# Performance work log

Hardware: AMD Instinct MI355X
Metric: run time of the kernel (lower is better)

## Reference

```python
import jax, jax.numpy as jnp
import numpy as np

B, NPG, K, F_IN, H = 64, 256, 100, 5, 128  # graphs, nodes/graph, knn k, in feats, hidden
N = B * NPG
H2 = 6 * H
SLOPE = 0.01  # leaky_relu default
EPS = 1e-5    # batchnorm eps


def _leaky(x):
    return jnp.where(x > 0, x, SLOPE * x)


def _knn_edges(x):
    # knn_graph(x, K, batch), loop=False, flow=source_to_target: edges j->i for the
    # K nearest neighbors j of node i within the same graph.
    xb = x.reshape(B, NPG, F_IN)
    d2 = jnp.sum((xb[:, :, None, :] - xb[:, None, :, :]) ** 2, axis=-1)  # [B,NPG,NPG]
    d2 = d2 + jnp.eye(NPG, dtype=d2.dtype) * 1e10  # exclude self
    _, idx = jax.lax.top_k(-d2, K)  # [B,NPG,K] local neighbor ids
    offs = (jnp.arange(B) * NPG)[:, None, None]
    src = (idx + offs).reshape(-1)
    dst = jnp.broadcast_to(jnp.arange(NPG)[None, :, None] + offs, (B, NPG, K)).reshape(-1)
    return src, dst


def _tagconv(x, src, dst, norm, Ws, b):
    # PyG TAGConv: out = sum_k lin_k(L^k x), L = D^-1/2 A D^-1/2 (no self loops)
    out = x @ Ws[0]
    h = x
    for k in range(1, Ws.shape[0]):
        msg = h[src] * norm[:, None]                      # gather [E,F]
        h = jax.ops.segment_sum(msg, dst, num_segments=N)  # scatter-add
        out = out + h @ Ws[k]
    return out + b


def _pool(x, batch):
    cnt = jax.ops.segment_sum(jnp.ones((N,), x.dtype), batch, num_segments=B)
    mean = jax.ops.segment_sum(x, batch, num_segments=B) / cnt[:, None]
    mx = jax.ops.segment_max(x, batch, num_segments=B)
    return jnp.concatenate([mean, mx], axis=1)  # [B, 2F]


def reference(x, batch, conv1_w, conv1_b, conv2_w, conv2_b, conv3_w, conv3_b,
              bn_gamma, bn_beta, lin_w, lin_b, out_w, out_b):
    src, dst = _knn_edges(x)
    # gcn_norm: deg from target side, symmetric scaling
    deg = jax.ops.segment_sum(jnp.ones(src.shape, x.dtype), dst, num_segments=N)
    dinv = jnp.where(deg > 0, deg ** -0.5, 0.0)
    norm = dinv[src] * dinv[dst]

    h = _leaky(_tagconv(x, src, dst, norm, conv1_w, conv1_b))
    p1 = _pool(h, batch)
    h = _leaky(_tagconv(h, src, dst, norm, conv2_w, conv2_b))
    p2 = _pool(h, batch)
    h = _leaky(_tagconv(h, src, dst, norm, conv3_w, conv3_b))
    p3 = _pool(h, batch)

    g = jnp.concatenate([p1, p2, p3], axis=1)  # [B, 768]
    mu = jnp.mean(g, axis=0)
    var = jnp.mean((g - mu) ** 2, axis=0)
    g = (g - mu) * jax.lax.rsqrt(var + EPS) * bn_gamma + bn_beta

    for i in range(5):
        g = _leaky(g @ lin_w[i] + lin_b[i])
    return (g @ out_w + out_b).reshape(-1)


def setup_inputs() -> dict:
    key = jax.random.key(0)
    ks = jax.random.split(key, 16)
    x = jax.random.normal(ks[0], (N, F_IN), jnp.float32)
    batch = jnp.repeat(jnp.arange(B, dtype=jnp.int32), NPG)

    def w(k, shape, fan_in):
        return jax.random.normal(k, shape, jnp.float32) * (1.0 / np.sqrt(fan_in))

    return {
        "x": x, "batch": batch,
        "conv1_w": w(ks[1], (3, F_IN, H), F_IN), "conv1_b": jnp.zeros((H,), jnp.float32),
        "conv2_w": w(ks[2], (3, H, H), H), "conv2_b": jnp.zeros((H,), jnp.float32),
        "conv3_w": w(ks[3], (3, H, H), H), "conv3_b": jnp.zeros((H,), jnp.float32),
        "bn_gamma": jnp.ones((H2,), jnp.float32), "bn_beta": jnp.zeros((H2,), jnp.float32),
        "lin_w": w(ks[4], (5, H2, H2), H2), "lin_b": jnp.zeros((5, H2), jnp.float32),
        "out_w": w(ks[5], (H2, 1), H2), "out_b": jnp.zeros((1,), jnp.float32),
    }
```

## Files before the change

### kernel.cpp

```cpp
#include <hip/hip_runtime.h>
#include <hip/hip_bf16.h>
#include <math.h>

#define NN 16384
#define BB 64
#define NPG 256
#define KNN 100
#define FIN 5
#define HH 128
#define H2 768
#define SLOPE 0.01f

typedef __bf16 bf16x8 __attribute__((ext_vector_type(8)));
typedef float f32x4 __attribute__((ext_vector_type(4)));

__device__ __forceinline__ int detect_bf(const void* gamma) {
    return ((const unsigned*)gamma)[0] == 0x3F803F80u;
}
__device__ __forceinline__ float loadin(const void* p, size_t i, int bf) {
    return bf ? __bfloat162float(((const __hip_bfloat16*)p)[i]) : ((const float*)p)[i];
}
template <typename T>
__device__ __forceinline__ float ldT(const T* p, size_t i) { return (float)p[i]; }
template <>
__device__ __forceinline__ float ldT<__hip_bfloat16>(const __hip_bfloat16* p, size_t i) {
    return __bfloat162float(p[i]);
}
__device__ __forceinline__ float4 ldT4(const float* p) { return *(const float4*)p; }
__device__ __forceinline__ float4 ldT4(const __hip_bfloat16* p) {
    ushort4 u = *(const ushort4*)p;
    return make_float4(__uint_as_float((unsigned)u.x << 16),
                       __uint_as_float((unsigned)u.y << 16),
                       __uint_as_float((unsigned)u.z << 16),
                       __uint_as_float((unsigned)u.w << 16));
}
__device__ __forceinline__ void stage_chunk(float* dst, const float* src, int n, int t) {
    const float4* s = (const float4*)src;
    float4* d = (float4*)dst;
    int n4 = n >> 2;
    for (int i = t; i < n4; i += 256) d[i] = s[i];
}
__device__ __forceinline__ void stage_chunk(float* dst, const __hip_bfloat16* src, int n, int t) {
    const ushort4* s = (const ushort4*)src;
    int n4 = n >> 2;
    for (int i = t; i < n4; i += 256) {
        ushort4 u = s[i];
        dst[i * 4 + 0] = __uint_as_float((unsigned)u.x << 16);
        dst[i * 4 + 1] = __uint_as_float((unsigned)u.y << 16);
        dst[i * 4 + 2] = __uint_as_float((unsigned)u.z << 16);
        dst[i * 4 + 3] = __uint_as_float((unsigned)u.w << 16);
    }
}

__device__ __forceinline__ unsigned enc_f(float f) {
    unsigned u = __float_as_uint(f);
    return (u & 0x80000000u) ? ~u : (u | 0x80000000u);
}
__device__ __forceinline__ float dec_f(unsigned u) {
    return __uint_as_float((u & 0x80000000u) ? (u & 0x7FFFFFFFu) : ~u);
}
__device__ __forceinline__ unsigned f2bf(float f) {
    unsigned u = __float_as_uint(f);
    unsigned r = 0x7fffu + ((u >> 16) & 1u);
    return (u + r) >> 16;
}
__device__ __forceinline__ void split1(float x, unsigned short& h, unsigned short& l) {
    unsigned u = __float_as_uint(x);
    unsigned hb = u & 0xFFFF0000u;
    h = (unsigned short)(hb >> 16);
    float rem = x - __uint_as_float(hb);
    l = (unsigned short)f2bf(rem);
}

__global__ __launch_bounds__(256) void knn_kernel(const void* __restrict__ x_in,
                                                  const void* gamma,
                                                  unsigned char* __restrict__ nbr,
                                                  float* __restrict__ g,
                                                  float* __restrict__ outf,
                                                  unsigned* __restrict__ done) {
    int blk = blockIdx.x;
    int bf = detect_bf(gamma);
    int b = blk >> 6;
    int wave = threadIdx.x >> 6;
    int lane = threadIdx.x & 63;
    int il = ((blk & 63) << 2) + wave;
    {
        int gi = blk * 256 + threadIdx.x;
        if (blk < 192 && gi < BB * H2) {
            int cm = gi & 255;
            g[gi] = (cm < 128) ? 0.0f : __uint_as_float(0x007FFFFFu);
        }
        if (blk == 0 && threadIdx.x < BB) {
            outf[threadIdx.x] = 0.0f;
            done[threadIdx.x] = 0u;
        }
    }
    __shared__ float xg[FIN * NPG];
    for (int idx = threadIdx.x; idx < NPG * FIN; idx += 256) {
        int node = idx / FIN, c = idx - node * FIN;
        xg[c * NPG + node] = loadin(x_in, (size_t)b * NPG * FIN + idx, bf);
    }
    __syncthreads();
    float dq[4] = {0.f, 0.f, 0.f, 0.f};
    #pragma unroll
    for (int c = 0; c < FIN; ++c) {
        float xi = xg[c * NPG + il];
        float4 xv = *(const float4*)&xg[c * NPG + lane * 4];
        float d0 = xi - xv.x, d1 = xi - xv.y, d2 = xi - xv.z, d3 = xi - xv.w;
        dq[0] += d0 * d0; dq[1] += d1 * d1; dq[2] += d2 * d2; dq[3] += d3 * d3;
    }
    unsigned long long kq[4];
    #pragma unroll
    for (int q = 0; q < 4; ++q) {
        int e = lane * 4 + q;
        float dd = (e == il) ? 1e30f : dq[q];
        kq[q] = ((unsigned long long)__float_as_uint(dd) << 32) | (unsigned)e;
    }
    #pragma unroll
    for (int kk = 2; kk <= NPG; kk <<= 1) {
        #pragma unroll
        for (int j = kk >> 1; j > 0; j >>= 1) {
            unsigned long long nk[4];
            if (j >= 4) {
                int lj = j >> 2;
                #pragma unroll
                for (int q = 0; q < 4; ++q) {
                    unsigned long long pk = __shfl_xor(kq[q], lj, 64);
                    int e = lane * 4 + q;
                    bool keepmin = (((e & j) == 0) == ((e & kk) == 0));
                    unsigned long long mn = kq[q] < pk ? kq[q] : pk;
                    unsigned long long mx = kq[q] < pk ? pk : kq[q];
                    nk[q] = keepmin ? mn : mx;
                }
            } else {
                #pragma unroll
                for (int q = 0; q < 4; ++q) {
                    unsigned long long pk = kq[q ^ j];
                    int e = lane * 4 + q;
                    bool keepmin = (((e & j) == 0) == ((e & kk) == 0));
                    unsigned long long mn = kq[q] < pk ? kq[q] : pk;
                    unsigned long long mx = kq[q] < pk ? pk : kq[q];
                    nk[q] = keepmin ? mn : mx;
                }
            }
            kq[0] = nk[0]; kq[1] = nk[1]; kq[2] = nk[2]; kq[3] = nk[3];
        }
    }
    if (lane < 25) {
        uchar4 o = make_uchar4((unsigned char)kq[0], (unsigned char)kq[1],
                               (unsigned char)kq[2], (unsigned char)kq[3]);
        *(uchar4*)&nbr[(size_t)(b * NPG + il) * KNN + lane * 4] = o;
    }
}

__global__ void agg5x2_kernel(const void* __restrict__ x_in, const void* gamma,
                              const unsigned char* __restrict__ nbr,
                              float* __restrict__ t5a, float* __restrict__ t5b, float nrm) {
    int b = blockIdx.x, i = threadIdx.x;
    int bf = detect_bf(gamma);
    __shared__ float xs[NPG * FIN];
    __shared__ float ys[NPG * FIN];
    for (int idx = threadIdx.x; idx < NPG * FIN; idx += 256)
        xs[idx] = loadin(x_in, (size_t)b * NPG * FIN + idx, bf);
    __syncthreads();
    const unsigned char* nb = nbr + (size_t)(b * NPG + i) * KNN;
    float a0=0.f, a1=0.f, a2=0.f, a3=0.f, a4=0.f;
    for (int k = 0; k < KNN; ++k) {
        int base = (int)nb[k] * FIN;
        a0 += xs[base+0]; a1 += xs[base+1]; a2 += xs[base+2];
        a3 += xs[base+3]; a4 += xs[base+4];
    }
    a0 *= nrm; a1 *= nrm; a2 *= nrm; a3 *= nrm; a4 *= nrm;
    size_t o = (size_t)(b * NPG + i) * FIN;
    t5a[o+0] = a0; t5a[o+1] = a1; t5a[o+2] = a2; t5a[o+3] = a3; t5a[o+4] = a4;
    ys[i*FIN+0] = a0; ys[i*FIN+1] = a1; ys[i*FIN+2] = a2;
    ys[i*FIN+3] = a3; ys[i*FIN+4] = a4;
    __syncthreads();
    a0=0.f; a1=0.f; a2=0.f; a3=0.f; a4=0.f;
    for (int k = 0; k < KNN; ++k) {
        int base = (int)nb[k] * FIN;
        a0 += ys[base+0]; a1 += ys[base+1]; a2 += ys[base+2];
        a3 += ys[base+3]; a4 += ys[base+4];
    }
    t5b[o+0] = nrm*a0; t5b[o+1] = nrm*a1; t5b[o+2] = nrm*a2;
    t5b[o+3] = nrm*a3; t5b[o+4] = nrm*a4;
}

__global__ __launch_bounds__(256) void agg_mfma_kernel(
        const float* __restrict__ hin, const unsigned char* __restrict__ nbr,
        float* __restrict__ hout, float nrm) {
    __shared__ __align__(16) unsigned short At[64 * 256];
    __shared__ __align__(16) unsigned short Ht[64 * 256];
    int t = threadIdx.x;
    int gph = blockIdx.x;
    int m0 = blockIdx.y * 64;
    int c0 = blockIdx.z * 64;
    {
        uint4 zz = make_uint4(0u, 0u, 0u, 0u);
        uint4* za = (uint4*)At;
        #pragma unroll
        for (int i = 0; i < 8; ++i) za[t + i * 256] = zz;
    }
    __syncthreads();
    for (int it = t; it < NPG * 4; it += 256) {
        int nq = it >> 4, c4 = it & 15;
        const float* src = &hin[((size_t)(gph * NPG + nq * 4)) * HH + c0 + c4 * 4];
        float4 v0 = *(const float4*)(src);
        float4 v1 = *(const float4*)(src + HH);
        float4 v2 = *(const float4*)(src + 2 * HH);
        float4 v3 = *(const float4*)(src + 3 * HH);
        #pragma unroll
        for (int j = 0; j < 4; ++j) {
            int c = c4 * 4 + j;
            ushort4 pk;
            pk.x = (unsigned short)f2bf((&v0.x)[j]);
            pk.y = (unsigned short)f2bf((&v1.x)[j]);
            pk.z = (unsigned short)f2bf((&v2.x)[j]);
            pk.w = (unsigned short)f2bf((&v3.x)[j]);
            unsigned off = (unsigned)((c * 512 + nq * 8) ^ ((c & 7) << 4));
            *(ushort4*)((char*)Ht + off) = pk;
        }
    }
    {
        int r = t >> 2, q = t & 3;
        const unsigned char* nb = nbr + ((size_t)(gph * NPG + m0 + r)) * KNN + q * 25;
        unsigned rbase = (unsigned)(r * 512);
        unsigned rswz = (unsigned)((r & 7) << 4);
        for (int j = 0; j < 25; ++j) {
            int col = (int)nb[j];
            *(unsigned short*)((char*)At + ((rbase + col * 2) ^ rswz)) = 0x3F80u;
        }
    }
    __syncthreads();
    int wv = t >> 6, lane = t & 63;
    unsigned kgb = (unsigned)((lane >> 4) * 16);
    unsigned swz = (unsigned)((lane & 7) << 4);
    unsigned abase = (unsigned)((wv * 16 + (lane & 15)) * 512) + kgb;
    f32x4 acc[4];
    #pragma unroll
    for (int nt = 0; nt < 4; ++nt) acc[nt] = (f32x4){0.f, 0.f, 0.f, 0.f};
    #pragma unroll
    for (int ks = 0; ks < 8; ++ks) {
        bf16x8 a = *(const bf16x8*)((char*)At + ((abase + ks * 64) ^ swz));
        #pragma unroll
        for (int nt = 0; nt < 4; ++nt) {
            unsigned bb = (unsigned)((nt * 16 + (lane & 15)) * 512) + kgb + ks * 64;
            bf16x8 bv = *(const bf16x8*)((char*)Ht + (bb ^ swz));
            acc[nt] = __builtin_amdgcn_mfma_f32_16x16x32_bf16(a, bv, acc[nt], 0, 0, 0);
        }
    }
    int rbase2 = m0 + wv * 16 + (lane >> 4) * 4;
    #pragma unroll
    for (int nt = 0; nt < 4; ++nt) {
        int col = c0 + nt * 16 + (lane & 15);
        #pragma unroll
        for (int reg = 0; reg < 4; ++reg) {
            int node = gph * NPG + rbase2 + reg;
            hout[(size_t)node * HH + col] = acc[nt][reg] * nrm;
        }
    }
}

__device__ __forceinline__ void pool_epilogue(float* g, int b, int gc0, int cg, int rp,
                                              float* sv, float* mv) {
    #pragma unroll
    for (int mask = 1; mask < 16; mask <<= 1) {
        #pragma unroll
        for (int i = 0; i < 8; ++i) {
            sv[i] += __shfl_xor(sv[i], mask);
            mv[i] = fmaxf(mv[i], __shfl_xor(mv[i], mask));
        }
    }
    if (rp == 0) {
        #pragma unroll
        for (int i = 0; i < 8; ++i) {
            atomicAdd(&g[(size_t)b * H2 + gc0 + cg * 8 + i], sv[i]);
            atomicMax((unsigned*)&g[(size_t)b * H2 + gc0 + HH + cg * 8 + i], enc_f(mv[i]));
        }
    }
}

template <typename T>
__device__ __forceinline__ void tagmm5_body(
        const T* __restrict__ X0raw, const float* __restrict__ X1,
        const float* __restrict__ X2,
        const T* __restrict__ W, const T* __restrict__ bias,
        float* __restrict__ O, float* g, float* Ws, float* Xs) {
    int t = threadIdx.x;
    int r0 = blockIdx.x * 16;
    int r = t & 15, cg = t >> 4;
    float acc[8] = {0.f,0.f,0.f,0.f,0.f,0.f,0.f,0.f};
    for (int h = 0; h < 3; ++h) {
        stage_chunk(Ws, W + (size_t)h * FIN * HH, FIN * HH, t);
        for (int idx = t; idx < 16 * FIN; idx += 256) {
            int rr = idx / FIN, k = idx - rr * FIN;
            size_t src = (size_t)(r0 + rr) * FIN + k;
            Xs[rr * 9 + k] = (h == 0) ? ldT(X0raw, src)
                           : (h == 1) ? X1[src] : X2[src];
        }
        __syncthreads();
        #pragma unroll
        for (int k = 0; k < FIN; ++k) {
            float xv = Xs[r * 9 + k];
            const float4 wa = *(const float4*)&Ws[k * HH + cg * 8];
            const float4 wb = *(const float4*)&Ws[k * HH + cg * 8 + 4];
            acc[0] += xv * wa.x; acc[1] += xv * wa.y;
            acc[2] += xv * wa.z; acc[3] += xv * wa.w;
            acc[4] += xv * wb.x; acc[5] += xv * wb.y;
            acc[6] += xv * wb.z; acc[7] += xv * wb.w;
        }
        __syncthreads();
    }
    size_t orow = (size_t)(r0 + r) * HH + cg * 8;
    float sv[8], mv[8];
    #pragma unroll
    for (int m = 0; m < 8; ++m) {
        float v = acc[m] + ldT(bias, cg * 8 + m);
        v = v > 0.f ? v : SLOPE * v;
        O[orow + m] = v;
        sv[m] = v * (1.0f / NPG);
        mv[m] = v;
    }
    pool_epilogue(g, r0 >> 8, 0, cg, r, sv, mv);
}

__global__ __launch_bounds__(256) void tagmm5_kernel(
        const void* X0raw, const float* X1, const float* X2,
        const void* W, const void* bias, float* O, float* g, const void* gamma) {
    __shared__ float Ws[FIN * HH];
    __shared__ float Xs[16 * 9];
    if (detect_bf(gamma))
        tagmm5_body<__hip_bfloat16>((const __hip_bfloat16*)X0raw, X1, X2,
                                    (const __hip_bfloat16*)W,
                                    (const __hip_bfloat16*)bias, O, g, Ws, Xs);
    else
        tagmm5_body<float>((const float*)X0raw, X1, X2, (const float*)W,
                           (const float*)bias, O, g, Ws, Xs);
}

template <typename T>
__device__ __forceinline__ void tagmm_mfma_body(
        const float* __restrict__ X0, const float* __restrict__ X1,
        const float* __restrict__ X2,
        const T* __restrict__ W, const T* __restrict__ bias,
        float* __restrict__ O, float* g, int gcp,
        unsigned short* Xhi, unsigned short* Xlo,
        unsigned short* Whi, unsigned short* Wlo, float* pred) {
    int t = threadIdx.x;
    int m0 = blockIdx.x * 64;
    int gc0 = blockIdx.y * 64;
    int wv = t >> 6, lane = t & 63;
    const float* Xh[3] = {X0, X1, X2};
    f32x4 acc[4];
    #pragma unroll
    for (int nt = 0; nt < 4; ++nt) acc[nt] = (f32x4){0.f, 0.f, 0.f, 0.f};
    unsigned kgb = (unsigned)((lane >> 4) * 16);
    unsigned swz = (unsigned)((lane & 7) << 4);
    unsigned abase = (unsigned)((wv * 16 + (lane & 15)) * 256) + kgb;
    for (int h = 0; h < 3; ++h) {
        const float* X = Xh[h];
        for (int i = t; i < 2048; i += 256) {
            int row = i >> 5, c4 = i & 31;
            float4 v = *(const float4*)&X[(size_t)(m0 + row) * HH + c4 * 4];
            unsigned off = (unsigned)((row * 256 + c4 * 8) ^ ((row & 7) << 4));
            ushort4 h4, l4;
            split1(v.x, h4.x, l4.x); split1(v.y, h4.y, l4.y);
            split1(v.z, h4.z, l4.z); split1(v.w, h4.w, l4.w);
            *(ushort4*)((char*)Xhi + off) = h4;
            *(ushort4*)((char*)Xlo + off) = l4;
        }
        const T* Wg = W + ((size_t)h * HH) * HH + gc0;
        for (int i = t; i < 512; i += 256) {
            int kq = i >> 4, n4 = i & 15;
            int k0 = kq * 4;
            float4 v0 = ldT4(Wg + (size_t)(k0 + 0) * HH + n4 * 4);
            float4 v1 = ldT4(Wg + (size_t)(k0 + 1) * HH + n4 * 4);
            float4 v2 = ldT4(Wg + (size_t)(k0 + 2) * HH + n4 * 4);
            float4 v3 = ldT4(Wg + (size_t)(k0 + 3) * HH + n4 * 4);
            #pragma unroll
            for (int j = 0; j < 4; ++j) {
                int n = n4 * 4 + j;
                ushort4 hv, lv;
                split1((&v0.x)[j], hv.x, lv.x);
                split1((&v1.x)[j], hv.y, lv.y);
                split1((&v2.x)[j], hv.z, lv.z);
                split1((&v3.x)[j], hv.w, lv.w);
                unsigned off = (unsigned)((n * 256 + k0 * 2) ^ ((n & 7) << 4));
                *(ushort4*)((char*)Whi + off) = hv;
                *(ushort4*)((char*)Wlo + off) = lv;
            }
        }
        __syncthreads();
        #pragma unroll
        for (int ks = 0; ks < 4; ++ks) {
            bf16x8 ah = *(const bf16x8*)((char*)Xhi + ((abase + ks * 64) ^ swz));
            bf16x8 al = *(const bf16x8*)((char*)Xlo + ((abase + ks * 64) ^ swz));
            #pragma unroll
            for (int nt = 0; nt < 4; ++nt) {
                unsigned bb = ((unsigned)((nt * 16 + (lane & 15)) * 256) + kgb + ks * 64) ^ swz;
                bf16x8 bh = *(const bf16x8*)((char*)Whi + bb);
                bf16x8 bl = *(const bf16x8*)((char*)Wlo + bb);
                acc[nt] = __builtin_amdgcn_mfma_f32_16x16x32_bf16(ah, bh, acc[nt], 0, 0, 0);
                acc[nt] = __builtin_amdgcn_mfma_f32_16x16x32_bf16(ah, bl, acc[nt], 0, 0, 0);
                acc[nt] = __builtin_amdgcn_mfma_f32_16x16x32_bf16(al, bh, acc[nt], 0, 0, 0);
            }
        }
        __syncthreads();
    }
    int b = m0 >> 8;
    int grow0 = m0 + wv * 16 + (lane >> 4) * 4;
    float* psum = pred;
    float* pmax = pred + 256;
    #pragma unroll
    for (int nt = 0; nt < 4; ++nt) {
        int ncol = nt * 16 + (lane & 15);
        float bv = ldT(bias, gc0 + ncol);
        float cs = 0.f, cm = -INFINITY;
        #pragma unroll
        for (int reg = 0; reg < 4; ++reg) {
            float v = acc[nt][reg] + bv;
            v = v > 0.f ? v : SLOPE * v;
            O[(size_t)(grow0 + reg) * HH + gc0 + ncol] = v;
            cs += v;
            cm = fmaxf(cm, v);
        }
        cs += __shfl_xor(cs, 16); cs += __shfl_xor(cs, 32);
        cm = fmaxf(cm, __shfl_xor(cm, 16)); cm = fmaxf(cm, __shfl_xor(cm, 32));
        if (lane < 16) {
            psum[wv * 64 + ncol] = cs;
            pmax[wv * 64 + ncol] = cm;
        }
    }
    __syncthreads();
    if (t < 64) {
        float s = psum[t] + psum[64 + t] + psum[128 + t] + psum[192 + t];
        float m = fmaxf(fmaxf(pmax[t], pmax[64 + t]), fmaxf(pmax[128 + t], pmax[192 + t]));
        atomicAdd(&g[(size_t)b * H2 + gcp + gc0 + t], s * (1.0f / NPG));
        atomicMax((unsigned*)&g[(size_t)b * H2 + gcp + HH + gc0 + t], enc_f(m));
    }
}

__global__ __launch_bounds__(256) void tagmm_mfma_kernel(
        const float* X0, const float* X1, const float* X2,
        const void* W, const void* bias, float* O, float* g, int gcp, const void* gamma) {
    __shared__ __align__(16) unsigned short Xhi[64 * 128];
    __shared__ __align__(16) unsigned short Xlo[64 * 128];
    __shared__ __align__(16) unsigned short Whi[64 * 128];
    __shared__ __align__(16) unsigned short Wlo[64 * 128];
    __shared__ float pred[512];
    if (detect_bf(gamma))
        tagmm_mfma_body<__hip_bfloat16>(X0, X1, X2, (const __hip_bfloat16*)W,
                                        (const __hip_bfloat16*)bias, O, g, gcp,
                                        Xhi, Xlo, Whi, Wlo, pred);
    else
        tagmm_mfma_body<float>(X0, X1, X2, (const float*)W, (const float*)bias,
                               O, g, gcp, Xhi, Xlo, Whi, Wlo, pred);
}

__global__ void bn_split_kernel(const float* __restrict__ g, const void* gamma,
                                const void* beta, unsigned short* __restrict__ ghi,
                                unsigned short* __restrict__ glo) {
    int c = blockIdx.x * 128 + threadIdx.x;
    int bf = detect_bf(gamma);
    int ismax = (c & 255) >= 128;
    float s = 0.f, s2 = 0.f;
    #pragma unroll 8
    for (int b = 0; b < BB; ++b) {
        float raw = g[(size_t)b * H2 + c];
        float x = ismax ? dec_f(__float_as_uint(raw)) : raw;
        s += x; s2 += x * x;
    }
    float mu = s * (1.0f / BB);
    float var = fmaxf(s2 * (1.0f / BB) - mu * mu, 0.f);
    float rs = 1.0f / sqrtf(var + 1e-5f);
    float ga = loadin(gamma, c, bf), be = loadin(beta, c, bf);
    #pragma unroll 8
    for (int b = 0; b < BB; ++b) {
        float raw = g[(size_t)b * H2 + c];
        float x = ismax ? dec_f(__float_as_uint(raw)) : raw;
        float y = (x - mu) * rs * ga + be;
        unsigned short h, l;
        split1(y, h, l);
        ghi[(size_t)b * H2 + c] = h;
        glo[(size_t)b * H2 + c] = l;
    }
}

template <typename T>
__device__ __forceinline__ void mlp_mfma2_body(
        const unsigned short* __restrict__ Xhi_g, const unsigned short* __restrict__ Xlo_g,
        const T* __restrict__ W, const T* __restrict__ bias,
        unsigned short* __restrict__ Ohi, unsigned short* __restrict__ Olo,
        const T* __restrict__ ow, const T* __restrict__ ob,
        float* __restrict__ outf, unsigned* __restrict__ done, void* out, int bf,
        unsigned short* Xhi, unsigned short* Xlo,
        unsigned short* Whi, unsigned short* Wlo, float* red4, float* red) {
    int t = threadIdx.x;
    int col0 = blockIdx.x * 16;
    int wv = t >> 6, lane = t & 63;
    f32x4 acc[4];
    #pragma unroll
    for (int mt = 0; mt < 4; ++mt) acc[mt] = (f32x4){0.f, 0.f, 0.f, 0.f};
    unsigned swz = (unsigned)((lane & 7) << 4);
    unsigned kgb = (unsigned)(wv * 64 + (lane >> 4) * 16);
    for (int ch = 0; ch < 6; ++ch) {
        int k0 = ch * 128;
        #pragma unroll
        for (int u = 0; u < 4; ++u) {
            int i = t + u * 256;
            int row = i >> 4, grp = i & 15;
            uint4 vh = *(const uint4*)&Xhi_g[(size_t)row * H2 + k0 + grp * 8];
            uint4 vl = *(const uint4*)&Xlo_g[(size_t)row * H2 + k0 + grp * 8];
            unsigned off = (unsigned)((row * 256 + grp * 16) ^ ((row & 7) << 4));
            *(uint4*)((char*)Xhi + off) = vh;
            *(uint4*)((char*)Xlo + off) = vl;
        }
        if (t < 128) {
            int kq = t >> 2, n4 = t & 3;
            int kb = k0 + kq * 4;
            float4 v0 = ldT4(W + (size_t)(kb + 0) * H2 + col0 + n4 * 4);
            float4 v1 = ldT4(W + (size_t)(kb + 1) * H2 + col0 + n4 * 4);
            float4 v2 = ldT4(W + (size_t)(kb + 2) * H2 + col0 + n4 * 4);
            float4 v3 = ldT4(W + (size_t)(kb + 3) * H2 + col0 + n4 * 4);
            #pragma unroll
            for (int j = 0; j < 4; ++j) {
                int n = n4 * 4 + j;
                ushort4 hv, lv;
                split1((&v0.x)[j], hv.x, lv.x);
                split1((&v1.x)[j], hv.y, lv.y);
                split1((&v2.x)[j], hv.z, lv.z);
                split1((&v3.x)[j], hv.w, lv.w);
                unsigned off = (unsigned)((n * 256 + kq * 8) ^ ((n & 7) << 4));
                *(ushort4*)((char*)Whi + off) = hv;
                *(ushort4*)((char*)Wlo + off) = lv;
            }
        }
        __syncthreads();
        unsigned bb = ((unsigned)((lane & 15) * 256) + kgb) ^ swz;
        bf16x8 bh = *(const bf16x8*)((char*)Whi + bb);
        bf16x8 bl = *(const bf16x8*)((char*)Wlo + bb);
        #pragma unroll
        for (int mt = 0; mt < 4; ++mt) {
            unsigned ab = ((unsigned)((mt * 16 + (lane & 15)) * 256) + kgb) ^ swz;
            bf16x8 ah = *(const bf16x8*)((char*)Xhi + ab);
            bf16x8 al = *(const bf16x8*)((char*)Xlo + ab);
            acc[mt] = __builtin_amdgcn_mfma_f32_16x16x32_bf16(ah, bh, acc[mt], 0, 0, 0);
            acc[mt] = __builtin_amdgcn_mfma_f32_16x16x32_bf16(ah, bl, acc[mt], 0, 0, 0);
            acc[mt] = __builtin_amdgcn_mfma_f32_16x16x32_bf16(al, bh, acc[mt], 0, 0, 0);
            acc[mt] = __builtin_amdgcn_mfma_f32_16x16x32_bf16(al, bl, acc[mt], 0, 0, 0);
        }
        __syncthreads();
    }
    #pragma unroll
    for (int mt = 0; mt < 4; ++mt) {
        int row = mt * 16 + (lane >> 4) * 4;
        #pragma unroll
        for (int reg = 0; reg < 4; ++reg)
            red4[wv * 1024 + (row + reg) * 16 + (lane & 15)] = acc[mt][reg];
    }
    __syncthreads();
    int row = t >> 2, cq = t & 3;
    const float4 s0 = *(const float4*)&red4[t * 4];
    const float4 s1 = *(const float4*)&red4[1024 + t * 4];
    const float4 s2 = *(const float4*)&red4[2048 + t * 4];
    const float4 s3 = *(const float4*)&red4[3072 + t * 4];
    float vout[4];
    #pragma unroll
    for (int j = 0; j < 4; ++j) {
        float v = (&s0.x)[j] + (&s1.x)[j] + (&s2.x)[j] + (&s3.x)[j]
                + ldT(bias, col0 + cq * 4 + j);
        vout[j] = v > 0.f ? v : SLOPE * v;
    }
    if (Ohi) {
        ushort4 hv, lv;
        split1(vout[0], hv.x, lv.x); split1(vout[1], hv.y, lv.y);
        split1(vout[2], hv.z, lv.z); split1(vout[3], hv.w, lv.w);
        *(ushort4*)&Ohi[(size_t)row * H2 + col0 + cq * 4] = hv;
        *(ushort4*)&Olo[(size_t)row * H2 + col0 + cq * 4] = lv;
    } else {
        float p = 0.f;
        #pragma unroll
        for (int j = 0; j < 4; ++j)
            p += vout[j] * ldT(ow, col0 + cq * 4 + j);
        red[cq * 64 + row] = p;
        __syncthreads();
        if (t < BB) {
            float s = red[t] + red[64 + t] + red[128 + t] + red[192 + t];
            atomicAdd(&outf[t], s);
            __threadfence();
            unsigned ticket = atomicAdd(&done[t], 1u);
            if (ticket == 47u) {
                __threadfence();
                float v = outf[t] + ldT(ob, 0);
                if (bf) ((__hip_bfloat16*)out)[t] = __float2bfloat16(v);
                else    ((float*)out)[t] = v;
            }
        }
    }
}

__global__ __launch_bounds__(256) void mlp_mfma2_kernel(
        const unsigned short* Xhi_g, const unsigned short* Xlo_g,
        const void* W, size_t woff, const void* bias, size_t boff,
        unsigned short* Ohi, unsigned short* Olo,
        const void* ow, const void* ob, float* outf, unsigned* done, void* out,
        const void* gamma) {
    __shared__ __align__(16) unsigned short Xhi[64 * 128];
    __shared__ __align__(16) unsigned short Xlo[64 * 128];
    __shared__ __align__(16) unsigned short Whi[16 * 128];
    __shared__ __align__(16) unsigned short Wlo[16 * 128];
    __shared__ float red4[4 * 1024];
    __shared__ float red[256];
    if (detect_bf(gamma))
        mlp_mfma2_body<__hip_bfloat16>(Xhi_g, Xlo_g,
                                       (const __hip_bfloat16*)W + woff,
                                       (const __hip_bfloat16*)bias + boff, Ohi, Olo,
                                       (const __hip_bfloat16*)ow, (const __hip_bfloat16*)ob,
                                       outf, done, out, 1,
                                       Xhi, Xlo, Whi, Wlo, red4, red);
    else
        mlp_mfma2_body<float>(Xhi_g, Xlo_g, (const float*)W + woff,
                              (const float*)bias + boff, Ohi, Olo,
                              (const float*)ow, (const float*)ob,
                              outf, done, out, 0,
                              Xhi, Xlo, Whi, Wlo, red4, red);
}

extern "C" void kernel_launch(void* const* d_in, const int* in_sizes, int n_in,
                              void* d_out, int out_size, void* d_ws, size_t ws_size,
                              hipStream_t stream) {
    const void* x_in = d_in[0];
    const void* c1w = d_in[2];  const void* c1b = d_in[3];
    const void* c2w = d_in[4];  const void* c2b = d_in[5];
    const void* c3w = d_in[6];  const void* c3b = d_in[7];
    const void* gam = d_in[8];  const void* bet = d_in[9];
    const void* lw  = d_in[10]; const void* lb  = d_in[11];
    const void* ow  = d_in[12]; const void* obb = d_in[13];

    char* w = (char*)d_ws;
    unsigned char* nbr = (unsigned char*)w;  w += (size_t)NN * KNN;
    float* t5a = (float*)w;                  w += (size_t)NN * FIN * 4;
    float* t5b = (float*)w;                  w += (size_t)NN * FIN * 4;
    float* bufA = (float*)w;                 w += (size_t)NN * HH * 4;
    float* bufB = (float*)w;                 w += (size_t)NN * HH * 4;
    float* bufC = (float*)w;                 w += (size_t)NN * HH * 4;
    float* bufD = (float*)w;                 w += (size_t)NN * HH * 4;
    float* g = (float*)w;                    w += (size_t)BB * H2 * 4;
    float* mA = (float*)w;                   w += (size_t)BB * H2 * 4;
    float* mB = (float*)w;                   w += (size_t)BB * H2 * 4;
    float* outf = (float*)w;                 w += (size_t)BB * 4;
    unsigned* done = (unsigned*)w;           w += (size_t)BB * 4;
    unsigned short* Ahi = (unsigned short*)mA;
    unsigned short* Alo = Ahi + (size_t)BB * H2;
    unsigned short* Bhi = (unsigned short*)mB;
    unsigned short* Blo = Bhi + (size_t)BB * H2;

    float dinv = 1.0f / sqrtf((float)KNN);
    float nrm = dinv * dinv;

    knn_kernel<<<NN / 4, 256, 0, stream>>>(x_in, gam, nbr, g, outf, done);

    dim3 aggm_grid(BB, 4, 2);
    dim3 tag_grid(NN / 64, 2);

    agg5x2_kernel<<<BB, 256, 0, stream>>>(x_in, gam, nbr, t5a, t5b, nrm);
    tagmm5_kernel<<<NN / 16, 256, 0, stream>>>(x_in, t5a, t5b, c1w, c1b, bufA, g, gam);

    agg_mfma_kernel<<<aggm_grid, 256, 0, stream>>>(bufA, nbr, bufB, nrm);
    agg_mfma_kernel<<<aggm_grid, 256, 0, stream>>>(bufB, nbr, bufC, nrm);
    tagmm_mfma_kernel<<<tag_grid, 256, 0, stream>>>(bufA, bufB, bufC, c2w, c2b,
                                                    bufD, g, 256, gam);

    agg_mfma_kernel<<<aggm_grid, 256, 0, stream>>>(bufD, nbr, bufA, nrm);
    agg_mfma_kernel<<<aggm_grid, 256, 0, stream>>>(bufA, nbr, bufB, nrm);
    tagmm_mfma_kernel<<<tag_grid, 256, 0, stream>>>(bufD, bufA, bufB, c3w, c3b,
                                                    bufC, g, 512, gam);

    bn_split_kernel<<<6, 128, 0, stream>>>(g, gam, bet, Ahi, Alo);

    mlp_mfma2_kernel<<<48, 256, 0, stream>>>(Ahi, Alo, lw, (size_t)0 * H2 * H2,
                                             lb, 0 * H2, Bhi, Blo,
                                             nullptr, nullptr, nullptr, nullptr,
                                             nullptr, gam);
    mlp_mfma2_kernel<<<48, 256, 0, stream>>>(Bhi, Blo, lw, (size_t)1 * H2 * H2,
                                             lb, 1 * H2, Ahi, Alo,
                                             nullptr, nullptr, nullptr, nullptr,
                                             nullptr, gam);
    mlp_mfma2_kernel<<<48, 256, 0, stream>>>(Ahi, Alo, lw, (size_t)2 * H2 * H2,
                                             lb, 2 * H2, Bhi, Blo,
                                             nullptr, nullptr, nullptr, nullptr,
                                             nullptr, gam);
    mlp_mfma2_kernel<<<48, 256, 0, stream>>>(Bhi, Blo, lw, (size_t)3 * H2 * H2,
                                             lb, 3 * H2, Ahi, Alo,
                                             nullptr, nullptr, nullptr, nullptr,
                                             nullptr, gam);
    mlp_mfma2_kernel<<<48, 256, 0, stream>>>(Ahi, Alo, lw, (size_t)4 * H2 * H2,
                                             lb, 4 * H2, nullptr, nullptr,
                                             ow, obb, outf, done, d_out, gam);
}
```

Measured before the change: 285.4 us.

## Replace bitonic sort with radix-select threshold for kNN neighbor selection

Replaces the full 256-element bitonic sort per query node (64-bit key shuffles) with a bitwise radix select. A ballot and popcount per bit finds the K-th smallest distance. Neighbors below the threshold, plus ties taken up to the quota in index order, are then compacted into the output in index order rather than sorted order. This removes the many shuffle and compare stages of the sort. The kernel becomes a 31-iteration ballot loop plus byte-wise scattered stores, and downstream code must not depend on neighbor order.

```diff
diff --git a/kernel.cpp b/kernel.cpp
--- a/kernel.cpp
+++ b/kernel.cpp
@@ -109,47 +109,48 @@
         float d0 = xi - xv.x, d1 = xi - xv.y, d2 = xi - xv.z, d3 = xi - xv.w;
         dq[0] += d0 * d0; dq[1] += d1 * d1; dq[2] += d2 * d2; dq[3] += d3 * d3;
     }
-    unsigned long long kq[4];
+    unsigned dk[4];
     #pragma unroll
     for (int q = 0; q < 4; ++q) {
         int e = lane * 4 + q;
         float dd = (e == il) ? 1e30f : dq[q];
-        kq[q] = ((unsigned long long)__float_as_uint(dd) << 32) | (unsigned)e;
-    }
-    #pragma unroll
-    for (int kk = 2; kk <= NPG; kk <<= 1) {
-        #pragma unroll
-        for (int j = kk >> 1; j > 0; j >>= 1) {
-            unsigned long long nk[4];
-            if (j >= 4) {
-                int lj = j >> 2;
-                #pragma unroll
-                for (int q = 0; q < 4; ++q) {
-                    unsigned long long pk = __shfl_xor(kq[q], lj, 64);
-                    int e = lane * 4 + q;
-                    bool keepmin = (((e & j) == 0) == ((e & kk) == 0));
-                    unsigned long long mn = kq[q] < pk ? kq[q] : pk;
-                    unsigned long long mx = kq[q] < pk ? pk : kq[q];
-                    nk[q] = keepmin ? mn : mx;
-                }
-            } else {
-                #pragma unroll
-                for (int q = 0; q < 4; ++q) {
-                    unsigned long long pk = kq[q ^ j];
-                    int e = lane * 4 + q;
-                    bool keepmin = (((e & j) == 0) == ((e & kk) == 0));
-                    unsigned long long mn = kq[q] < pk ? kq[q] : pk;
-                    unsigned long long mx = kq[q] < pk ? pk : kq[q];
-                    nk[q] = keepmin ? mn : mx;
-                }
-            }
-            kq[0] = nk[0]; kq[1] = nk[1]; kq[2] = nk[2]; kq[3] = nk[3];
-        }
-    }
-    if (lane < 25) {
-        uchar4 o = make_uchar4((unsigned char)kq[0], (unsigned char)kq[1],
-                               (unsigned char)kq[2], (unsigned char)kq[3]);
-        *(uchar4*)&nbr[(size_t)(b * NPG + il) * KNN + lane * 4] = o;
+        dk[q] = __float_as_uint(dd);
+    }
+    unsigned P = 0;
+    for (int bit = 30; bit >= 0; --bit) {
+        unsigned cand = P | (1u << bit);
+        int c = __popcll(__ballot(dk[0] < cand)) + __popcll(__ballot(dk[1] < cand))
+              + __popcll(__ballot(dk[2] < cand)) + __popcll(__ballot(dk[3] < cand));
+        if (c < KNN) P = cand;
+    }
+    unsigned long long meq[4];
+    int n_less = 0;
+    #pragma unroll
+    for (int q = 0; q < 4; ++q) {
+        n_less += __popcll(__ballot(dk[q] < P));
+        meq[q] = __ballot(dk[q] == P);
+    }
+    int quota = KNN - n_less;
+    unsigned long long below = (1ull << lane) - 1ull;
+    int run_eq = __popcll(meq[0] & below) + __popcll(meq[1] & below)
+               + __popcll(meq[2] & below) + __popcll(meq[3] & below);
+    bool sel[4];
+    #pragma unroll
+    for (int q = 0; q < 4; ++q) {
+        int iseq = (int)((meq[q] >> lane) & 1ull);
+        sel[q] = (dk[q] < P) || (iseq && run_eq < quota);
+        run_eq += iseq;
+    }
+    unsigned long long msel[4];
+    #pragma unroll
+    for (int q = 0; q < 4; ++q) msel[q] = __ballot(sel[q]);
+    int pos = __popcll(msel[0] & below) + __popcll(msel[1] & below)
+            + __popcll(msel[2] & below) + __popcll(msel[3] & below);
+    unsigned char* nb = &nbr[(size_t)(b * NPG + il) * KNN];
+    #pragma unroll
+    for (int q = 0; q < 4; ++q) {
+        if (sel[q]) nb[pos] = (unsigned char)(lane * 4 + q);
+        pos += sel[q] ? 1 : 0;
     }
 }
 
```

New measurement: 264.1 us (median of 3 runs). 1.08x faster.
